# Kernel optimization log

Hardware: AMD Instinct MI355X
Metric: run time of the kernel (lower is better)

Reference implementation:

```python
import jax, jax.numpy as jnp
import numpy as np

QMIN, QMAX = -128.0, 127.0


def setup_inputs() -> dict:
    key = jax.random.key(0)
    kx, kw, kb = jax.random.split(key, 3)
    B, S, K, M = 4, 2048, 4096, 4096
    x = jax.random.normal(kx, (B, S, K), dtype=jnp.float32)
    bound = 1.0 / np.sqrt(K)  # kaiming_uniform(a=sqrt(5)) -> U(-1/sqrt(fan_in), 1/sqrt(fan_in))
    W = jax.random.uniform(kw, (M, K), dtype=jnp.float32, minval=-bound, maxval=bound)
    b = jax.random.uniform(kb, (M,), dtype=jnp.float32, minval=-bound, maxval=bound)
    return {"x": x, "W": W, "b": b}


def _quant_weights_rowwise(W):
    # symmetric per-row int8: scale = absmax/127
    absmax = jnp.max(jnp.abs(W), axis=1, keepdims=True)  # [M,1]
    scale = jnp.where(absmax > 0, absmax / QMAX, 1.0)
    Wq = jnp.clip(jnp.round(W / scale), QMIN, QMAX)
    return Wq, scale


def _quant_acts_per_token(X):
    # asymmetric per-token (per column of X.t()) int8 with zero-point
    xmin = jnp.min(X, axis=1, keepdims=True)  # [N,1]
    xmax = jnp.max(X, axis=1, keepdims=True)
    rng = xmax - xmin
    scale = jnp.where(rng > 0, rng / (QMAX - QMIN), 1.0)
    zp = jnp.clip(jnp.round(QMIN - xmin / scale), QMIN, QMAX)
    Xq = jnp.clip(jnp.round(X / scale + zp), QMIN, QMAX)
    return Xq, scale, zp


def reference(x, W, b):
    B, S, K = x.shape
    X = x.reshape(-1, K)  # [N, K]
    Wq, row_scale = _quant_weights_rowwise(W)          # [M,K], [M,1]
    Xq, col_scale, zp = _quant_acts_per_token(X)       # [N,K], [N,1], [N,1]
    # fused dequant-GEMM: Y = ((Xq - zp) * col_scale) @ (Wq * row_scale).T
    Wdq = Wq * row_scale                               # [M,K]
    Xdq = (Xq - zp) * col_scale                        # [N,K]
    Y = jnp.einsum('nk,mk->nm', Xdq, Wdq) + b          # [N,M]
    return Y.reshape(B, S, -1)
```

## Files before the change

### kernel.cpp

```cpp
#include <hip/hip_runtime.h>
#include <stdint.h>


typedef __attribute__((ext_vector_type(4)))  int int4v;
typedef __attribute__((ext_vector_type(16))) int int16v;

__device__ __forceinline__ void async_load16(const void* g, void* l) {
    __builtin_amdgcn_global_load_lds(
        (const __attribute__((address_space(1))) void*)g,
        (__attribute__((address_space(3))) void*)l, 16, 0, 0);
}

__device__ __forceinline__ int quant_clip(float v) {
    return (int)fminf(fmaxf(rintf(v), -128.f), 127.f);
}

__global__ __launch_bounds__(256) void quant_kernel(
    const float* __restrict__ W, const float* __restrict__ X,
    int8_t* __restrict__ Wq, int8_t* __restrict__ Xq,
    float* __restrict__ row_scale, int* __restrict__ wsum,
    float* __restrict__ col_scale, int* __restrict__ zp, int M, int K) {
    const int blk  = blockIdx.x;
    const int tid  = threadIdx.x;
    const int lane = tid & 63;
    const int wv   = tid >> 6;
    __shared__ float sred0[4], sred1[4];
    __shared__ int   isum[4];

    if (blk < M) {
        const int row = blk;
        const float4* w4 = (const float4*)(W + (size_t)row * K);
        float4 vals[4];
        float amax = 0.f;
#pragma unroll
        for (int i = 0; i < 4; ++i) {
            float4 v = w4[tid + i * 256];
            vals[i] = v;
            amax = fmaxf(amax, fmaxf(fmaxf(fabsf(v.x), fabsf(v.y)),
                                     fmaxf(fabsf(v.z), fabsf(v.w))));
        }
#pragma unroll
        for (int off = 32; off > 0; off >>= 1)
            amax = fmaxf(amax, __shfl_down(amax, off, 64));
        if (lane == 0) sred0[wv] = amax;
        __syncthreads();
        amax = fmaxf(fmaxf(sred0[0], sred0[1]), fmaxf(sred0[2], sred0[3]));

        const float scale = (amax > 0.f) ? (amax / 127.f) : 1.f;
        const float inv   = 1.f / scale;

        int ssum = 0;
        int* wq32 = (int*)(Wq + (size_t)row * K);
#pragma unroll
        for (int i = 0; i < 4; ++i) {
            float4 v = vals[i];
            int q0 = quant_clip(v.x * inv);
            int q1 = quant_clip(v.y * inv);
            int q2 = quant_clip(v.z * inv);
            int q3 = quant_clip(v.w * inv);
            ssum += q0 + q1 + q2 + q3;
            wq32[tid + i * 256] =
                (q0 & 0xff) | ((q1 & 0xff) << 8) | ((q2 & 0xff) << 16) | ((q3 & 0xff) << 24);
        }
#pragma unroll
        for (int off = 32; off > 0; off >>= 1)
            ssum += __shfl_down(ssum, off, 64);
        if (lane == 0) isum[wv] = ssum;
        __syncthreads();
        if (tid == 0) {
            wsum[row] = isum[0] + isum[1] + isum[2] + isum[3];
            row_scale[row] = scale;
        }
    } else {
        const int row = blk - M;
        const float4* x4 = (const float4*)(X + (size_t)row * K);
        float4 vals[4];
        float vmin = 3.402823466e+38f, vmax = -3.402823466e+38f;
#pragma unroll
        for (int i = 0; i < 4; ++i) {
            float4 v = x4[tid + i * 256];
            vals[i] = v;
            vmin = fminf(vmin, fminf(fminf(v.x, v.y), fminf(v.z, v.w)));
            vmax = fmaxf(vmax, fmaxf(fmaxf(v.x, v.y), fmaxf(v.z, v.w)));
        }
#pragma unroll
        for (int off = 32; off > 0; off >>= 1) {
            vmin = fminf(vmin, __shfl_down(vmin, off, 64));
            vmax = fmaxf(vmax, __shfl_down(vmax, off, 64));
        }
        if (lane == 0) { sred0[wv] = vmin; sred1[wv] = vmax; }
        __syncthreads();
        vmin = fminf(fminf(sred0[0], sred0[1]), fminf(sred0[2], sred0[3]));
        vmax = fmaxf(fmaxf(sred1[0], sred1[1]), fmaxf(sred1[2], sred1[3]));

        const float rng   = vmax - vmin;
        const float scale = (rng > 0.f) ? (rng / 255.f) : 1.f;
        const float inv   = 1.f / scale;
        const float zpf   = fminf(fmaxf(rintf(-128.f - vmin * inv), -128.f), 127.f);

        int* xq32 = (int*)(Xq + (size_t)row * K);
#pragma unroll
        for (int i = 0; i < 4; ++i) {
            float4 v = vals[i];
            int q0 = quant_clip(v.x * inv + zpf);
            int q1 = quant_clip(v.y * inv + zpf);
            int q2 = quant_clip(v.z * inv + zpf);
            int q3 = quant_clip(v.w * inv + zpf);
            xq32[tid + i * 256] =
                (q0 & 0xff) | ((q1 & 0xff) << 8) | ((q2 & 0xff) << 16) | ((q3 & 0xff) << 24);
        }
        if (tid == 0) {
            col_scale[row] = scale;
            zp[row] = (int)zpf;
        }
    }
}

#define REGION(buf, mat, kh) (lds + ((((buf) * 2 + (mat)) * 2 + (kh)) << 14))

__device__ __forceinline__ void compute_half(
    const int8_t* Ar, const int8_t* Br,
    const int aoff[4], const int boff[2],
    const int half, const int sw4, int16v (&acc)[4][2]) {
    __builtin_amdgcn_s_setprio(1);
#pragma unroll
    for (int ss = 0; ss < 2; ++ss) {
        const int cc = ((((ss << 1) + half) ^ sw4) << 4);
        int4v a[4], b[2];
#pragma unroll
        for (int i = 0; i < 4; ++i)
            a[i] = *(const int4v*)(Ar + aoff[i] + cc);
#pragma unroll
        for (int j = 0; j < 2; ++j)
            b[j] = *(const int4v*)(Br + boff[j] + cc);
#pragma unroll
        for (int i = 0; i < 4; ++i)
#pragma unroll
            for (int j = 0; j < 2; ++j)
                acc[i][j] = __builtin_amdgcn_mfma_i32_32x32x32_i8(
                    a[i], b[j], acc[i][j], 0, 0, 0);
    }
    __builtin_amdgcn_s_setprio(0);
}

__global__ __launch_bounds__(512, 2) void gemm_i8_kernel(
    const int8_t* __restrict__ Xq, const int8_t* __restrict__ Wq,
    const float* __restrict__ cs, const int* __restrict__ zp,
    const float* __restrict__ rs, const int* __restrict__ wsum,
    const float* __restrict__ bias, float* __restrict__ out,
    int N, int M, int K) {
    __shared__ __align__(16) int8_t lds[131072];

    const int t    = threadIdx.x;
    const int wv   = t >> 6;
    const int lane = t & 63;
    const int r32  = lane & 31;
    const int half = lane >> 5;
    const int wn   = wv >> 2;
    const int wm   = wv & 3;

    const int nMB = M >> 8;
    const int per = ((M >> 8) * (N >> 8)) >> 3;
    const int lin = blockIdx.x;
    const int g   = (lin & 7) * per + (lin >> 3);
    const int m0  = (g % nMB) << 8;
    const int n0  = (g / nMB) << 8;

    const int NT = K >> 7;

    const int lrow   = (wv << 4) + (lane >> 2);
    const int srcOff = (((lane & 3) ^ ((lane >> 3) & 3)) << 4);
    const int8_t* gA0 = Xq + (size_t)(n0 + lrow) * K + srcOff;
    const int8_t* gA1 = Xq + (size_t)(n0 + 128 + lrow) * K + srcOff;
    const int8_t* gB0 = Wq + (size_t)(m0 + lrow) * K + srcOff;
    const int8_t* gB1 = Wq + (size_t)(m0 + 128 + lrow) * K + srcOff;
    const int wvOff = wv << 10;

    int aoff[4], boff[2];
#pragma unroll
    for (int i = 0; i < 4; ++i) aoff[i] = (((wn << 7) + i * 32 + r32) << 6);
#pragma unroll
    for (int j = 0; j < 2; ++j) boff[j] = (((wm << 6) + j * 32 + r32) << 6);
    const int sw4 = (r32 >> 1) & 3;

    int16v acc[4][2];
#pragma unroll
    for (int i = 0; i < 4; ++i)
#pragma unroll
        for (int j = 0; j < 2; ++j)
            acc[i][j] = (int16v)(0);

    {
        int8_t* r;
        r = REGION(0, 0, 0) + wvOff; async_load16(gA0, r);       async_load16(gA1, r + 8192);
        r = REGION(0, 1, 0) + wvOff; async_load16(gB0, r);       async_load16(gB1, r + 8192);
        r = REGION(0, 0, 1) + wvOff; async_load16(gA0 + 64, r);  async_load16(gA1 + 64, r + 8192);
        r = REGION(0, 1, 1) + wvOff; async_load16(gB0 + 64, r);  async_load16(gB1 + 64, r + 8192);
        r = REGION(1, 0, 0) + wvOff; async_load16(gA0 + 128, r); async_load16(gA1 + 128, r + 8192);
        r = REGION(1, 1, 0) + wvOff; async_load16(gB0 + 128, r); async_load16(gB1 + 128, r + 8192);
    }
    asm volatile("s_waitcnt vmcnt(8)" ::: "memory");
    __builtin_amdgcn_s_barrier();

    for (int tt = 0; tt < NT; ++tt) {
        const int buf = tt & 1;
        {
            const int tn = (tt + 1 < NT) ? tt + 1 : NT - 1;
            const int ko = (tn << 7) + 64;
            int8_t* r;
            r = REGION(buf ^ 1, 0, 1) + wvOff;
            async_load16(gA0 + ko, r); async_load16(gA1 + ko, r + 8192);
            r = REGION(buf ^ 1, 1, 1) + wvOff;
            async_load16(gB0 + ko, r); async_load16(gB1 + ko, r + 8192);

            compute_half(REGION(buf, 0, 0), REGION(buf, 1, 0), aoff, boff, half, sw4, acc);

            asm volatile("s_waitcnt vmcnt(8)" ::: "memory");
            __builtin_amdgcn_s_barrier();
        }
        {
            const int tn = (tt + 2 < NT) ? tt + 2 : NT - 1;
            const int ko = (tn << 7);
            int8_t* r;
            r = REGION(buf, 0, 0) + wvOff;
            async_load16(gA0 + ko, r); async_load16(gA1 + ko, r + 8192);
            r = REGION(buf, 1, 0) + wvOff;
            async_load16(gB0 + ko, r); async_load16(gB1 + ko, r + 8192);

            compute_half(REGION(buf, 0, 1), REGION(buf, 1, 1), aoff, boff, half, sw4, acc);

            asm volatile("s_waitcnt vmcnt(8)" ::: "memory");
            __builtin_amdgcn_s_barrier();
        }
    }

    int   mm[2];
    float rsv[2], bv[2];
    int   wsv[2];
#pragma unroll
    for (int j = 0; j < 2; ++j) {
        mm[j]  = m0 + (wm << 6) + j * 32 + r32;
        rsv[j] = rs[mm[j]];
        bv[j]  = bias[mm[j]];
        wsv[j] = wsum[mm[j]];
    }
#pragma unroll
    for (int i = 0; i < 4; ++i) {
        const int nbase = n0 + (wn << 7) + i * 32 + (half << 2);
#pragma unroll
        for (int reg = 0; reg < 16; ++reg) {
            const int n = nbase + (reg & 3) + 8 * (reg >> 2);
            const float csn = cs[n];
            const int   zpn = zp[n];
#pragma unroll
            for (int j = 0; j < 2; ++j) {
                const int ival = acc[i][j][reg] - zpn * wsv[j];
                out[(size_t)n * M + mm[j]] = csn * rsv[j] * (float)ival + bv[j];
            }
        }
    }
}

extern "C" void kernel_launch(void* const* d_in, const int* in_sizes, int n_in,
                              void* d_out, int out_size, void* d_ws, size_t ws_size,
                              hipStream_t stream) {
    const float* x = (const float*)d_in[0];
    const float* W = (const float*)d_in[1];
    const float* b = (const float*)d_in[2];
    float* out = (float*)d_out;

    const int M = in_sizes[2];
    const int K = in_sizes[1] / M;
    const int N = in_sizes[0] / K;

    int8_t* Xq = (int8_t*)d_ws;
    int8_t* Wq = Xq + (size_t)N * K;
    float* cs  = (float*)(Wq + (size_t)M * K);
    int* zps   = (int*)(cs + N);
    float* rs  = (float*)(zps + N);
    int* wsum  = (int*)(rs + M);

    quant_kernel<<<dim3(M + N), dim3(256), 0, stream>>>(
        W, x, Wq, Xq, rs, wsum, cs, zps, M, K);
    gemm_i8_kernel<<<dim3((M >> 8) * (N >> 8)), dim3(512), 0, stream>>>(
        Xq, Wq, cs, zps, rs, wsum, b, out, N, M, K);
}
```

Baseline: 409.9 us.

## Software-pipeline LDS fragment reads against MFMA with register double buffering

Restructures the int8 GEMM main loop into four quarter-steps. Each step reads the next set of A/B fragments from LDS into a second register set while the MFMAs consume the previous set, and the async global-to-LDS loads are split per matrix and interleaved between steps. The goal is to hide LDS read latency behind MFMA issue. The cost is more barriers per tile, more vector registers for the doubled fragments, and sched_barrier constraints that may limit compiler scheduling or occupancy.

```diff
diff --git a/kernel.cpp b/kernel.cpp
--- a/kernel.cpp
+++ b/kernel.cpp
@@ -118,28 +118,25 @@
 
 #define REGION(buf, mat, kh) (lds + ((((buf) * 2 + (mat)) * 2 + (kh)) << 14))
 
-__device__ __forceinline__ void compute_half(
-    const int8_t* Ar, const int8_t* Br,
-    const int aoff[4], const int boff[2],
-    const int half, const int sw4, int16v (&acc)[4][2]) {
+__device__ __forceinline__ void read6(int4v (&a)[4], int4v (&b)[2],
+                                      const int8_t* Ar, const int8_t* Br,
+                                      const int aoff[4], const int boff[2],
+                                      const int cc) {
+#pragma unroll
+    for (int i = 0; i < 4; ++i) a[i] = *(const int4v*)(Ar + aoff[i] + cc);
+#pragma unroll
+    for (int j = 0; j < 2; ++j) b[j] = *(const int4v*)(Br + boff[j] + cc);
+}
+
+__device__ __forceinline__ void mfma8(const int4v (&a)[4], const int4v (&b)[2],
+                                      int16v (&acc)[4][2]) {
     __builtin_amdgcn_s_setprio(1);
 #pragma unroll
-    for (int ss = 0; ss < 2; ++ss) {
-        const int cc = ((((ss << 1) + half) ^ sw4) << 4);
-        int4v a[4], b[2];
-#pragma unroll
-        for (int i = 0; i < 4; ++i)
-            a[i] = *(const int4v*)(Ar + aoff[i] + cc);
+    for (int i = 0; i < 4; ++i)
 #pragma unroll
         for (int j = 0; j < 2; ++j)
-            b[j] = *(const int4v*)(Br + boff[j] + cc);
-#pragma unroll
-        for (int i = 0; i < 4; ++i)
-#pragma unroll
-            for (int j = 0; j < 2; ++j)
-                acc[i][j] = __builtin_amdgcn_mfma_i32_32x32x32_i8(
-                    a[i], b[j], acc[i][j], 0, 0, 0);
-    }
+            acc[i][j] = __builtin_amdgcn_mfma_i32_32x32x32_i8(
+                a[i], b[j], acc[i][j], 0, 0, 0);
     __builtin_amdgcn_s_setprio(0);
 }
 
@@ -182,6 +179,8 @@
 #pragma unroll
     for (int j = 0; j < 2; ++j) boff[j] = (((wm << 6) + j * 32 + r32) << 6);
     const int sw4 = (r32 >> 1) & 3;
+    const int cc0 = ((half ^ sw4) << 4);
+    const int cc1 = (((2 + half) ^ sw4) << 4);
 
     int16v acc[4][2];
 #pragma unroll
@@ -202,36 +201,50 @@
     asm volatile("s_waitcnt vmcnt(8)" ::: "memory");
     __builtin_amdgcn_s_barrier();
 
+    int4v aA[4], bA[2], aB[4], bB[2];
+    read6(aA, bA, REGION(0, 0, 0), REGION(0, 1, 0), aoff, boff, cc0);
+
     for (int tt = 0; tt < NT; ++tt) {
         const int buf = tt & 1;
-        {
-            const int tn = (tt + 1 < NT) ? tt + 1 : NT - 1;
-            const int ko = (tn << 7) + 64;
-            int8_t* r;
-            r = REGION(buf ^ 1, 0, 1) + wvOff;
-            async_load16(gA0 + ko, r); async_load16(gA1 + ko, r + 8192);
-            r = REGION(buf ^ 1, 1, 1) + wvOff;
-            async_load16(gB0 + ko, r); async_load16(gB1 + ko, r + 8192);
-
-            compute_half(REGION(buf, 0, 0), REGION(buf, 1, 0), aoff, boff, half, sw4, acc);
-
-            asm volatile("s_waitcnt vmcnt(8)" ::: "memory");
-            __builtin_amdgcn_s_barrier();
-        }
-        {
-            const int tn = (tt + 2 < NT) ? tt + 2 : NT - 1;
-            const int ko = (tn << 7);
-            int8_t* r;
-            r = REGION(buf, 0, 0) + wvOff;
-            async_load16(gA0 + ko, r); async_load16(gA1 + ko, r + 8192);
-            r = REGION(buf, 1, 0) + wvOff;
-            async_load16(gB0 + ko, r); async_load16(gB1 + ko, r + 8192);
-
-            compute_half(REGION(buf, 0, 1), REGION(buf, 1, 1), aoff, boff, half, sw4, acc);
-
-            asm volatile("s_waitcnt vmcnt(8)" ::: "memory");
-            __builtin_amdgcn_s_barrier();
-        }
+        const int tn1 = (tt + 1 < NT) ? tt + 1 : NT - 1;
+        const int tn2 = (tt + 2 < NT) ? tt + 2 : NT - 1;
+        const int ko1 = (tn1 << 7) + 64;
+        const int ko2 = (tn2 << 7);
+        int8_t* r;
+
+        read6(aB, bB, REGION(buf, 0, 0), REGION(buf, 1, 0), aoff, boff, cc1);
+        r = REGION(buf ^ 1, 0, 1) + wvOff;
+        async_load16(gA0 + ko1, r); async_load16(gA1 + ko1, r + 8192);
+        __builtin_amdgcn_s_barrier();
+        __builtin_amdgcn_sched_barrier(0);
+        mfma8(aA, bA, acc);
+        asm volatile("s_waitcnt vmcnt(6)" ::: "memory");
+        __builtin_amdgcn_s_barrier();
+
+        read6(aA, bA, REGION(buf, 0, 1), REGION(buf, 1, 1), aoff, boff, cc0);
+        r = REGION(buf ^ 1, 1, 1) + wvOff;
+        async_load16(gB0 + ko1, r); async_load16(gB1 + ko1, r + 8192);
+        __builtin_amdgcn_s_barrier();
+        __builtin_amdgcn_sched_barrier(0);
+        mfma8(aB, bB, acc);
+        __builtin_amdgcn_s_barrier();
+
+        read6(aB, bB, REGION(buf, 0, 1), REGION(buf, 1, 1), aoff, boff, cc1);
+        r = REGION(buf, 0, 0) + wvOff;
+        async_load16(gA0 + ko2, r); async_load16(gA1 + ko2, r + 8192);
+        __builtin_amdgcn_s_barrier();
+        __builtin_amdgcn_sched_barrier(0);
+        mfma8(aA, bA, acc);
+        asm volatile("s_waitcnt vmcnt(6)" ::: "memory");
+        __builtin_amdgcn_s_barrier();
+
+        read6(aA, bA, REGION(buf ^ 1, 0, 0), REGION(buf ^ 1, 1, 0), aoff, boff, cc0);
+        r = REGION(buf, 1, 0) + wvOff;
+        async_load16(gB0 + ko2, r); async_load16(gB1 + ko2, r + 8192);
+        __builtin_amdgcn_s_barrier();
+        __builtin_amdgcn_sched_barrier(0);
+        mfma8(aB, bB, acc);
+        __builtin_amdgcn_s_barrier();
     }
 
     int   mm[2];
```

Result: no change. 405.9 us (-1.0%).
